# Kernel tuning notes

Measured on AMD Instinct MI355X. Metric: run time of the kernel, lower is better.

Reference implementation:

```python
import jax, jax.numpy as jnp
import numpy as np

RADIUS = 1
N_POINTS = 8


def lbp(x, radius=RADIUS, n_points=N_POINTS):
    """skimage-style 'default' LBP applied per pixel of an NCHW batch.

    For each of P points on a circle of radius R, bilinearly sample the
    neighbor (zero outside the image, matching skimage's constant mode),
    compare >= center, and bit-pack with weights 2**p.
    Offsets follow skimage: row = -R*sin(theta), col = R*cos(theta).
    """
    B, C, H, W = x.shape
    angles = 2.0 * np.pi * np.arange(n_points) / n_points
    drs = np.round(-radius * np.sin(angles), 8)
    dcs = np.round(radius * np.cos(angles), 8)
    pad = int(np.ceil(radius)) + 1
    xp = jnp.pad(x, ((0, 0), (0, 0), (pad, pad), (pad, pad)))  # zeros outside

    code = jnp.zeros_like(x)
    for p in range(n_points):
        dr, dc = float(drs[p]), float(dcs[p])
        r0, c0 = int(np.floor(dr)), int(np.floor(dc))
        fr, fc = dr - r0, dc - c0  # fractional parts in [0,1)

        def win(ri, ci):
            rs, cs = pad + r0 + ri, pad + c0 + ci
            return jax.lax.slice(xp, (0, 0, rs, cs), (B, C, rs + H, cs + W))

        # bilinear sample of the shifted neighborhood (constant-0 boundary)
        v = ((1 - fr) * (1 - fc) * win(0, 0)
             + (1 - fr) * fc * win(0, 1)
             + fr * (1 - fc) * win(1, 0)
             + fr * fc * win(1, 1))
        code = code + float(2 ** p) * (v >= x).astype(x.dtype)
    return code


def setup_inputs() -> dict:
    key = jax.random.key(0)
    x = jax.random.uniform(key, (16, 64, 224, 224), dtype=jnp.float32)
    return {"x": x}


def reference(x):
    return lbp(x)
```

## Files before the change

### kernel.cpp

```cpp
#include <hip/hip_runtime.h>
#include <math.h>

#define HH 224
#define WW 224
#define TOTAL (16 * 64 * 224 * 224)

struct LbpWeights {
    float w1[4];
    float w3[4];
    float w5[4];
    float w7[4];
};

__global__ __launch_bounds__(256) void lbp_kernel(const float* __restrict__ x,
                                                  float* __restrict__ out,
                                                  LbpWeights wt) {
    int idx = blockIdx.x * 256 + threadIdx.x;
    if (idx >= TOTAL) return;

    int c = idx % WW;
    int t = idx / WW;
    int r = t % HH;

    const float* p1 = x + idx;

    bool rm = (r > 0), rp = (r < HH - 1);
    bool cm = (c > 0), cp = (c < WW - 1);

    float n00 = (rm && cm) ? p1[-WW - 1] : 0.0f;
    float n01 = rm         ? p1[-WW]     : 0.0f;
    float n02 = (rm && cp) ? p1[-WW + 1] : 0.0f;
    float n10 = cm         ? p1[-1]      : 0.0f;
    float n11 =              p1[0];
    float n12 = cp         ? p1[1]       : 0.0f;
    float n20 = (rp && cm) ? p1[WW - 1]  : 0.0f;
    float n21 = rp         ? p1[WW]      : 0.0f;
    float n22 = (rp && cp) ? p1[WW + 1]  : 0.0f;

    float v1, v3, v5, v7;
    {
#pragma clang fp contract(off)
        v1 = ((wt.w1[0] * n01 + wt.w1[1] * n02) + wt.w1[2] * n11) + wt.w1[3] * n12;
        v3 = ((wt.w3[0] * n00 + wt.w3[1] * n01) + wt.w3[2] * n10) + wt.w3[3] * n11;
        v5 = ((wt.w5[0] * n10 + wt.w5[1] * n11) + wt.w5[2] * n20) + wt.w5[3] * n21;
        v7 = ((wt.w7[0] * n11 + wt.w7[1] * n12) + wt.w7[2] * n21) + wt.w7[3] * n22;
    }

    int m = 0;
    m |= (n12 >= n11) ? 1   : 0;
    m |= (v1  >= n11) ? 2   : 0;
    m |= (n01 >= n11) ? 4   : 0;
    m |= (v3  >= n11) ? 8   : 0;
    m |= (n10 >= n11) ? 16  : 0;
    m |= (v5  >= n11) ? 32  : 0;
    m |= (n21 >= n11) ? 64  : 0;
    m |= (v7  >= n11) ? 128 : 0;

    out[idx] = (float)m;
}

extern "C" void kernel_launch(void* const* d_in, const int* in_sizes, int n_in,
                              void* d_out, int out_size, void* d_ws, size_t ws_size,
                              hipStream_t stream) {
    (void)in_sizes; (void)n_in; (void)d_ws; (void)ws_size; (void)out_size;
    const float* x = (const float*)d_in[0];
    float* out = (float*)d_out;

    LbpWeights wt;
    float* slots[4] = {wt.w1, wt.w3, wt.w5, wt.w7};
    const int diag_p[4] = {1, 3, 5, 7};
    for (int i = 0; i < 4; i++) {
        int p = diag_p[i];
        double ang = (2.0 * M_PI * (double)p) / 8.0;
        double dr = rint(-sin(ang) * 1e8) / 1e8;
        double dc = rint( cos(ang) * 1e8) / 1e8;
        double r0 = floor(dr), c0 = floor(dc);
        double fr = dr - r0, fc = dc - c0;
        slots[i][0] = (float)((1.0 - fr) * (1.0 - fc));
        slots[i][1] = (float)((1.0 - fr) * fc);
        slots[i][2] = (float)(fr * (1.0 - fc));
        slots[i][3] = (float)(fr * fc);
    }

    const int total = TOTAL;
    const int block = 256;
    const int grid = (total + block - 1) / block;
    lbp_kernel<<<grid, block, 0, stream>>>(x, out, wt);
}
```

Before: 410.2 us.

## Compute 4x4 output tile per thread with float4 loads and register reuse

```diff
diff --git a/kernel.cpp b/kernel.cpp
--- a/kernel.cpp
+++ b/kernel.cpp
@@ -3,7 +3,10 @@
 
 #define HH 224
 #define WW 224
-#define TOTAL (16 * 64 * 224 * 224)
+#define PLANES (16 * 64)
+#define TILES_X (WW / 4)
+#define TILES_PER_PLANE (TILES_X * (HH / 4))
+#define TOTAL_THREADS (PLANES * TILES_PER_PLANE)
 
 struct LbpWeights {
     float w1[4];
@@ -15,48 +18,67 @@
 __global__ __launch_bounds__(256) void lbp_kernel(const float* __restrict__ x,
                                                   float* __restrict__ out,
                                                   LbpWeights wt) {
-    int idx = blockIdx.x * 256 + threadIdx.x;
-    if (idx >= TOTAL) return;
+    int tid = blockIdx.x * 256 + threadIdx.x;
 
-    int c = idx % WW;
-    int t = idx / WW;
-    int r = t % HH;
+    int plane = tid / TILES_PER_PLANE;
+    int t = tid - plane * TILES_PER_PLANE;
+    int tr = t / TILES_X;
+    int tc = t - tr * TILES_X;
+    int r0 = tr * 4, c0 = tc * 4;
 
-    const float* p1 = x + idx;
+    const float* pb = x + (size_t)plane * (HH * WW);
 
-    bool rm = (r > 0), rp = (r < HH - 1);
-    bool cm = (c > 0), cp = (c < WW - 1);
-
-    float n00 = (rm && cm) ? p1[-WW - 1] : 0.0f;
-    float n01 = rm         ? p1[-WW]     : 0.0f;
-    float n02 = (rm && cp) ? p1[-WW + 1] : 0.0f;
-    float n10 = cm         ? p1[-1]      : 0.0f;
-    float n11 =              p1[0];
-    float n12 = cp         ? p1[1]       : 0.0f;
-    float n20 = (rp && cm) ? p1[WW - 1]  : 0.0f;
-    float n21 = rp         ? p1[WW]      : 0.0f;
-    float n22 = (rp && cp) ? p1[WW + 1]  : 0.0f;
-
-    float v1, v3, v5, v7;
-    {
-#pragma clang fp contract(off)
-        v1 = ((wt.w1[0] * n01 + wt.w1[1] * n02) + wt.w1[2] * n11) + wt.w1[3] * n12;
-        v3 = ((wt.w3[0] * n00 + wt.w3[1] * n01) + wt.w3[2] * n10) + wt.w3[3] * n11;
-        v5 = ((wt.w5[0] * n10 + wt.w5[1] * n11) + wt.w5[2] * n20) + wt.w5[3] * n21;
-        v7 = ((wt.w7[0] * n11 + wt.w7[1] * n12) + wt.w7[2] * n21) + wt.w7[3] * n22;
+    float a[6][6];
+    bool cm = (c0 > 0), cp = (c0 + 4 < WW);
+#pragma unroll
+    for (int i = 0; i < 6; i++) {
+        int rr = r0 - 1 + i;
+        if (rr >= 0 && rr < HH) {
+            const float* rp = pb + rr * WW + c0;
+            float4 v = *(const float4*)rp;
+            a[i][1] = v.x; a[i][2] = v.y; a[i][3] = v.z; a[i][4] = v.w;
+            a[i][0] = cm ? rp[-1] : 0.0f;
+            a[i][5] = cp ? rp[4]  : 0.0f;
+        } else {
+#pragma unroll
+            for (int k = 0; k < 6; k++) a[i][k] = 0.0f;
+        }
     }
 
-    int m = 0;
-    m |= (n12 >= n11) ? 1   : 0;
-    m |= (v1  >= n11) ? 2   : 0;
-    m |= (n01 >= n11) ? 4   : 0;
-    m |= (v3  >= n11) ? 8   : 0;
-    m |= (n10 >= n11) ? 16  : 0;
-    m |= (v5  >= n11) ? 32  : 0;
-    m |= (n21 >= n11) ? 64  : 0;
-    m |= (v7  >= n11) ? 128 : 0;
+    float* ob = out + (size_t)plane * (HH * WW) + r0 * WW + c0;
 
-    out[idx] = (float)m;
+#pragma unroll
+    for (int j = 0; j < 4; j++) {
+        float res[4];
+#pragma unroll
+        for (int k = 0; k < 4; k++) {
+            float ctr = a[j + 1][k + 1];
+            float n00 = a[j][k],     n01 = a[j][k + 1],     n02 = a[j][k + 2];
+            float n10 = a[j + 1][k],                        n12 = a[j + 1][k + 2];
+            float n20 = a[j + 2][k], n21 = a[j + 2][k + 1], n22 = a[j + 2][k + 2];
+
+            float v1, v3, v5, v7;
+            {
+#pragma clang fp contract(off)
+                v1 = ((wt.w1[0] * n01 + wt.w1[1] * n02) + wt.w1[2] * ctr) + wt.w1[3] * n12;
+                v3 = ((wt.w3[0] * n00 + wt.w3[1] * n01) + wt.w3[2] * n10) + wt.w3[3] * ctr;
+                v5 = ((wt.w5[0] * n10 + wt.w5[1] * ctr) + wt.w5[2] * n20) + wt.w5[3] * n21;
+                v7 = ((wt.w7[0] * ctr + wt.w7[1] * n12) + wt.w7[2] * n21) + wt.w7[3] * n22;
+            }
+
+            int m = 0;
+            m |= (n12 >= ctr) ? 1   : 0;
+            m |= (v1  >= ctr) ? 2   : 0;
+            m |= (n01 >= ctr) ? 4   : 0;
+            m |= (v3  >= ctr) ? 8   : 0;
+            m |= (n10 >= ctr) ? 16  : 0;
+            m |= (v5  >= ctr) ? 32  : 0;
+            m |= (n21 >= ctr) ? 64  : 0;
+            m |= (v7  >= ctr) ? 128 : 0;
+            res[k] = (float)m;
+        }
+        *(float4*)(ob + j * WW) = make_float4(res[0], res[1], res[2], res[3]);
+    }
 }
 
 extern "C" void kernel_launch(void* const* d_in, const int* in_sizes, int n_in,
@@ -82,8 +104,7 @@
         slots[i][3] = (float)(fr * fc);
     }
 
-    const int total = TOTAL;
     const int block = 256;
-    const int grid = (total + block - 1) / block;
+    const int grid = TOTAL_THREADS / block;
     lbp_kernel<<<grid, block, 0, stream>>>(x, out, wt);
 }
```

New measurement: 371.8 us. 1.1x faster.
